# Kernel tuning notes

Measured on AMD Instinct MI355X. Metric: run time of the kernel, lower is better.

## Reference

```python
import jax, jax.numpy as jnp
import numpy as np

L, B, T, E, NH, HD, HID, V = 8, 2, 2048, 1024, 16, 64, 2816, 32000


def _rmsnorm(x, w, eps=1e-6):
    return w * (x * jax.lax.rsqrt(jnp.mean(x * x, axis=-1, keepdims=True) + eps))


def _rope(x, cos, sin):
    # x: [B,H,T,D]; cos/sin: [1,1,T,D/2]
    x1, x2 = jnp.split(x, 2, axis=-1)
    return jnp.concatenate([x1 * cos - x2 * sin, x1 * sin + x2 * cos], axis=-1)


def setup_inputs() -> dict:
    key = jax.random.key(0)
    ks = jax.random.split(key, 7)
    s = 0.02
    return {
        "idx": jax.random.randint(ks[0], (B, T), 0, V),
        "tok_emb": jax.random.normal(ks[1], (V, E), dtype=jnp.float32) * s,
        "qkv_w": jax.random.normal(ks[2], (L, 3 * E, E), dtype=jnp.float32) * s,
        "proj_w": jax.random.normal(ks[3], (L, E, E), dtype=jnp.float32) * s,
        "w1": jax.random.normal(ks[4], (L, HID, E), dtype=jnp.float32) * s,
        "w2": jax.random.normal(ks[5], (L, HID, E), dtype=jnp.float32) * s,
        "w3": jax.random.normal(ks[6], (L, E, HID), dtype=jnp.float32) * s,
        "norm1_w": jnp.ones((L, E), dtype=jnp.float32),
        "norm2_w": jnp.ones((L, E), dtype=jnp.float32),
        "norm_f_w": jnp.ones((E,), dtype=jnp.float32),
    }


def reference(idx, tok_emb, qkv_w, proj_w, w1, w2, w3, norm1_w, norm2_w, norm_f_w):
    x = tok_emb[idx]  # [B,T,E]
    # RoPE cache (start_pos=0, no kv cache -> prefill path)
    half = HD // 2
    inv_freq = 1.0 / (10000.0 ** (jnp.arange(half, dtype=jnp.float32) / half))
    pos = jnp.arange(T, dtype=jnp.float32)
    freqs = pos[:, None] * inv_freq[None, :]  # [T, D/2]
    cos = jnp.cos(freqs)[None, None]
    sin = jnp.sin(freqs)[None, None]
    causal = jnp.tril(jnp.ones((T, T), dtype=bool))
    scale = 1.0 / np.sqrt(HD).astype(np.float32)

    for l in range(L):
        # attention block
        h = _rmsnorm(x, norm1_w[l])
        qkv = h @ qkv_w[l].T  # [B,T,3E]
        q, k, v = jnp.split(qkv, 3, axis=-1)
        q = q.reshape(B, T, NH, HD).transpose(0, 2, 1, 3)
        k = k.reshape(B, T, NH, HD).transpose(0, 2, 1, 3)
        v = v.reshape(B, T, NH, HD).transpose(0, 2, 1, 3)
        q = _rope(q, cos, sin)
        k = _rope(k, cos, sin)
        att = jnp.einsum('bhqd,bhkd->bhqk', q, k) * scale
        att = jnp.where(causal, att, -jnp.inf)
        att = jax.nn.softmax(att, axis=-1)
        o = jnp.einsum('bhqk,bhkd->bhqd', att, v)
        o = o.transpose(0, 2, 1, 3).reshape(B, T, E)
        x = x + o @ proj_w[l].T
        # SwiGLU MLP
        h = _rmsnorm(x, norm2_w[l])
        x = x + (jax.nn.silu(h @ w1[l].T) * (h @ w2[l].T)) @ w3[l].T

    x = _rmsnorm(x, norm_f_w)
    logits = x @ tok_emb.T  # tied lm_head
    return logits
```

## Files before the change

kernel.cpp:

```cpp
#include <hip/hip_runtime.h>

#define GLOBAL_AS __attribute__((address_space(1)))
#define LDS_AS __attribute__((address_space(3)))

typedef unsigned short u16;
typedef unsigned int u32;
typedef __attribute__((ext_vector_type(4))) float f32x4;
typedef __attribute__((ext_vector_type(8))) short bf16x8;

#define TT 2048
#define EE 1024
#define NHH 16
#define HDD 64
#define HIDD 2816
#define VV 32000
#define MM 4096

__device__ __forceinline__ u16 f2bf(float f) {
  u32 u = __builtin_bit_cast(u32, f);
  u += 0x7fffu + ((u >> 16) & 1u);
  return (u16)(u >> 16);
}
__device__ __forceinline__ float bf2f(u16 v) {
  return __builtin_bit_cast(float, (u32)v << 16);
}


__global__ __launch_bounds__(256) void castbf_k(const float* __restrict__ in,
                                                u16* __restrict__ o, long n4) {
  const long i = (long)blockIdx.x * 256 + threadIdx.x;
  if (i >= n4) return;
  const float4 v = ((const float4*)in)[i];
  ((uint2*)o)[i] = make_uint2((u32)f2bf(v.x) | ((u32)f2bf(v.y) << 16),
                              (u32)f2bf(v.z) | ((u32)f2bf(v.w) << 16));
}

__global__ void ropetab_k(float* __restrict__ cosT, float* __restrict__ sinT) {
  const int t = blockIdx.x, j = threadIdx.x;
  const float inv = powf(10000.0f, -(float)j * (1.0f / 32.0f));
  const float f = (float)t * inv;
  cosT[t * 32 + j] = cosf(f);
  sinT[t * 32 + j] = sinf(f);
}

__global__ __launch_bounds__(256) void embed_k(const int* __restrict__ idx,
                                               const float* __restrict__ temb,
                                               float* __restrict__ x) {
  const int row = blockIdx.x;
  const int id = idx[row];
  ((float4*)(x + (size_t)row * EE))[threadIdx.x] =
      ((const float4*)(temb + (size_t)id * EE))[threadIdx.x];
}

__global__ __launch_bounds__(256) void rmsnorm_k(const float* __restrict__ x,
                                                 const float* __restrict__ w,
                                                 u16* __restrict__ o) {
  __shared__ float red[4];
  const int row = blockIdx.x, tid = threadIdx.x;
  const float4 v = ((const float4*)(x + (size_t)row * EE))[tid];
  float ss = v.x * v.x + v.y * v.y + v.z * v.z + v.w * v.w;
#pragma unroll
  for (int off = 32; off; off >>= 1) ss += __shfl_xor(ss, off, 64);
  if ((tid & 63) == 0) red[tid >> 6] = ss;
  __syncthreads();
  const float inv = rsqrtf((red[0] + red[1] + red[2] + red[3]) * (1.0f / 1024.0f) + 1e-6f);
  const float4 wv = ((const float4*)w)[tid];
  const u32 lo = (u32)f2bf(v.x * inv * wv.x) | ((u32)f2bf(v.y * inv * wv.y) << 16);
  const u32 hi = (u32)f2bf(v.z * inv * wv.z) | ((u32)f2bf(v.w * inv * wv.w) << 16);
  ((uint2*)(o + (size_t)row * EE))[tid] = make_uint2(lo, hi);
}

template <int OUTBF>
__global__ __launch_bounds__(512, 2) void gemm256p(const u16* __restrict__ A,
                                                   const u16* __restrict__ Bw,
                                                   float* __restrict__ C,
                                                   u16* __restrict__ C16,
                                                   const u16* __restrict__ G,
                                                   int N, int K) {
  __shared__ u16 lds[2 * 32768];
  const int t = threadIdx.x;
  const int lane = t & 63;
  const int wid = t >> 6;
  const int wr = wid >> 2;
  const int wc = wid & 3;
  const int l15 = lane & 15, lg = lane >> 4;
  const int bid = blockIdx.x;
  const int row0 = (bid & 15) << 8;
  const int col0 = (bid >> 4) << 8;
  const int NT = K >> 6;

  const int sr = t >> 3;
  const int su8 = (((t & 7) ^ (sr & 7)) << 3);
  const int t8 = t << 3;
  const u16* aG[4];
#pragma unroll
  for (int ga = 0; ga < 4; ++ga)
    aG[ga] = A + (size_t)(row0 + ga * 64 + sr) * K + su8;
  const u16* bG[4];
#pragma unroll
  for (int gb = 0; gb < 4; ++gb) {
    const int q = (gb * 2 + (sr >> 5)) & 3;
    const int nh = gb >> 1;
    bG[gb] = Bw + (size_t)(col0 + q * 64 + nh * 32 + (sr & 31)) * K + su8;
  }

  const int u0 = ((lg ^ (l15 & 7)) << 3);
  const int u1 = (((4 | lg) ^ (l15 & 7)) << 3);
  const int arow = (wr * 128 + l15) << 6;
  const int brow = 16384 + ((wc * 32 + l15) << 6);

  f32x4 acc[8][4] = {};

#define STA(nb, ga, k0n)                                                              \
  __builtin_amdgcn_global_load_lds((const GLOBAL_AS void*)(aG[ga] + (k0n)),           \
                                   (LDS_AS void*)((nb) + (ga)*4096 + t8), 16, 0, 0)
#define STB(nb, gb, k0n)                                                              \
  __builtin_amdgcn_global_load_lds((const GLOBAL_AS void*)(bG[gb] + (k0n)),           \
                                   (LDS_AS void*)((nb) + 16384 + (gb)*4096 + t8), 16, 0, 0)

  {
    u16* nb = lds;
    STA(nb, 0, 0); STA(nb, 2, 0);
    STB(nb, 0, 0); STB(nb, 1, 0);
    STB(nb, 2, 0); STB(nb, 3, 0);
    STA(nb, 1, 0); STA(nb, 3, 0);
  }

  bf16x8 af[4][2], bl[2][2], bh[2][2];

  for (int kt = 0; kt < NT; ++kt) {
    const bool st = (kt + 1 < NT);
    const int k0n = (kt + 1) << 6;
    const u16* cb = lds + (kt & 1) * 32768;
    u16* nb = lds + ((kt + 1) & 1) * 32768;

    asm volatile("s_waitcnt vmcnt(4)" ::: "memory");
    __builtin_amdgcn_s_barrier();
#pragma unroll
    for (int mi = 0; mi < 4; ++mi) {
      af[mi][0] = *(const bf16x8*)&cb[arow + mi * 1024 + u0];
      af[mi][1] = *(const bf16x8*)&cb[arow + mi * 1024 + u1];
    }
#pragma unroll
    for (int ni = 0; ni < 2; ++ni) {
      bl[ni][0] = *(const bf16x8*)&cb[brow + ni * 1024 + u0];
      bl[ni][1] = *(const bf16x8*)&cb[brow + ni * 1024 + u1];
    }
    if (st) { STA(nb, 0, k0n); STA(nb, 2, k0n); }
    __builtin_amdgcn_s_setprio(1);
#pragma unroll
    for (int mi = 0; mi < 4; ++mi)
#pragma unroll
      for (int ni = 0; ni < 2; ++ni) {
        acc[mi][ni] = __builtin_amdgcn_mfma_f32_16x16x32_bf16(af[mi][0], bl[ni][0], acc[mi][ni], 0, 0, 0);
        acc[mi][ni] = __builtin_amdgcn_mfma_f32_16x16x32_bf16(af[mi][1], bl[ni][1], acc[mi][ni], 0, 0, 0);
      }
    __builtin_amdgcn_s_setprio(0);

    if (st) { asm volatile("s_waitcnt vmcnt(4)" ::: "memory"); }
    else    { asm volatile("s_waitcnt vmcnt(2)" ::: "memory"); }
    __builtin_amdgcn_s_barrier();
#pragma unroll
    for (int ni = 0; ni < 2; ++ni) {
      bh[ni][0] = *(const bf16x8*)&cb[brow + 8192 + ni * 1024 + u0];
      bh[ni][1] = *(const bf16x8*)&cb[brow + 8192 + ni * 1024 + u1];
    }
    if (st) { STB(nb, 0, k0n); STB(nb, 1, k0n); }
    __builtin_amdgcn_s_setprio(1);
#pragma unroll
    for (int mi = 0; mi < 4; ++mi)
#pragma unroll
      for (int ni = 0; ni < 2; ++ni) {
        acc[mi][2 + ni] = __builtin_amdgcn_mfma_f32_16x16x32_bf16(af[mi][0], bh[ni][0], acc[mi][2 + ni], 0, 0, 0);
        acc[mi][2 + ni] = __builtin_amdgcn_mfma_f32_16x16x32_bf16(af[mi][1], bh[ni][1], acc[mi][2 + ni], 0, 0, 0);
      }
    __builtin_amdgcn_s_setprio(0);

    if (st) { asm volatile("s_waitcnt vmcnt(4)" ::: "memory"); }
    else    { asm volatile("s_waitcnt vmcnt(0)" ::: "memory"); }
    __builtin_amdgcn_s_barrier();
#pragma unroll
    for (int mi = 0; mi < 4; ++mi) {
      af[mi][0] = *(const bf16x8*)&cb[arow + (4 + mi) * 1024 + u0];
      af[mi][1] = *(const bf16x8*)&cb[arow + (4 + mi) * 1024 + u1];
    }
    if (st) { STB(nb, 2, k0n); STB(nb, 3, k0n); }
    __builtin_amdgcn_s_setprio(1);
#pragma unroll
    for (int mi = 0; mi < 4; ++mi)
#pragma unroll
      for (int ni = 0; ni < 2; ++ni) {
        acc[4 + mi][2 + ni] = __builtin_amdgcn_mfma_f32_16x16x32_bf16(af[mi][0], bh[ni][0], acc[4 + mi][2 + ni], 0, 0, 0);
        acc[4 + mi][2 + ni] = __builtin_amdgcn_mfma_f32_16x16x32_bf16(af[mi][1], bh[ni][1], acc[4 + mi][2 + ni], 0, 0, 0);
      }
    __builtin_amdgcn_s_setprio(0);

    if (st) { STA(nb, 1, k0n); STA(nb, 3, k0n); }
    __builtin_amdgcn_s_setprio(1);
#pragma unroll
    for (int mi = 0; mi < 4; ++mi)
#pragma unroll
      for (int ni = 0; ni < 2; ++ni) {
        acc[4 + mi][ni] = __builtin_amdgcn_mfma_f32_16x16x32_bf16(af[mi][0], bl[ni][0], acc[4 + mi][ni], 0, 0, 0);
        acc[4 + mi][ni] = __builtin_amdgcn_mfma_f32_16x16x32_bf16(af[mi][1], bl[ni][1], acc[4 + mi][ni], 0, 0, 0);
      }
    __builtin_amdgcn_s_setprio(0);
  }
#undef STA
#undef STB

#pragma unroll
  for (int m = 0; m < 8; ++m) {
    const int row = row0 + wr * 128 + m * 16 + lg * 4;
#pragma unroll
    for (int n = 0; n < 4; ++n) {
      const int col = col0 + wc * 64 + n * 16 + l15;
#pragma unroll
      for (int r = 0; r < 4; ++r) {
        const size_t o = (size_t)(row + r) * N + col;
        if (OUTBF == 0) {
          C[o] = acc[m][n][r];
        } else if (OUTBF == 1) {
          C16[o] = f2bf(acc[m][n][r]);
        } else {
          const float g = bf2f(G[o]);
          C16[o] = f2bf(g / (1.0f + __expf(-g)) * acc[m][n][r]);
        }
      }
    }
  }
}

template <int OUTBF>
__global__ __launch_bounds__(512, 2) void gemm128n(const u16* __restrict__ A,
                                                   const u16* __restrict__ Bw,
                                                   float* __restrict__ C,
                                                   const float* __restrict__ R,
                                                   const float* __restrict__ cosT,
                                                   const float* __restrict__ sinT,
                                                   u16* __restrict__ Qb,
                                                   u16* __restrict__ Kb,
                                                   u16* __restrict__ Vtb,
                                                   int N, int K) {
  __shared__ u16 lds[4 * 8192];
  const int t = threadIdx.x;
  const int lane = t & 63;
  const int wid = t >> 6;
  const int wr = wid & 3;
  const int wc = wid >> 2;
  const int l15 = lane & 15, lg = lane >> 4;
  const int bid = blockIdx.x;
  const int row0 = (bid & 31) << 7;
  const int col0 = (bid >> 5) << 7;
  const int NT = K >> 5;

  const int rA = t >> 2;
  const int usw = (((t & 3) ^ ((t >> 3) & 3)) << 3);
  const u16* sA = A + (size_t)(row0 + rA) * K + usw;
  const u16* sB = Bw + (size_t)(col0 + rA) * K + usw;
  const int dst = t << 3;

  const int e8 = ((lg ^ ((l15 >> 1) & 3)) << 3);
  const int aoff = (wr * 32 + l15) * 32 + e8;
  const int boff = 4096 + (wc * 64 + l15) * 32 + e8;

  f32x4 acc[2][4] = {};

  auto stage = [&](int kt) {
    u16* base = &lds[(kt & 3) * 8192];
    const size_t ko = (size_t)kt * 32;
    __builtin_amdgcn_global_load_lds((const GLOBAL_AS void*)(sA + ko),
                                     (LDS_AS void*)(base + dst), 16, 0, 0);
    __builtin_amdgcn_global_load_lds((const GLOBAL_AS void*)(sB + ko),
                                     (LDS_AS void*)(base + 4096 + dst), 16, 0, 0);
  };

  stage(0);
  stage(1);
  stage(2);

  for (int kt = 0; kt < NT; ++kt) {
    const int rem = NT - 1 - kt;
    if (rem >= 2) {
      asm volatile("s_waitcnt vmcnt(4)" ::: "memory");
    } else if (rem == 1) {
      asm volatile("s_waitcnt vmcnt(2)" ::: "memory");
    } else {
      asm volatile("s_waitcnt vmcnt(0)" ::: "memory");
    }
    __builtin_amdgcn_s_barrier();
    if (kt + 3 < NT) stage(kt + 3);
    const u16* base = &lds[(kt & 3) * 8192];
    bf16x8 af[2], bfv[4];
#pragma unroll
    for (int m = 0; m < 2; ++m) af[m] = *(const bf16x8*)&base[aoff + m * 512];
#pragma unroll
    for (int n = 0; n < 4; ++n) bfv[n] = *(const bf16x8*)&base[boff + n * 512];
    __builtin_amdgcn_s_setprio(1);
#pragma unroll
    for (int m = 0; m < 2; ++m)
#pragma unroll
      for (int n = 0; n < 4; ++n)
        acc[m][n] = __builtin_amdgcn_mfma_f32_16x16x32_bf16(af[m], bfv[n], acc[m][n], 0, 0, 0);
    __builtin_amdgcn_s_setprio(0);
  }

  if (OUTBF == 3) {
    const int reg = col0 >> 10;
    const int fb = col0 & 1023;
#pragma unroll
    for (int m = 0; m < 2; ++m) {
      const int row = row0 + wr * 32 + m * 16 + lg * 4;
      const int b = row >> 11, tbase = row & 2047;
      if (reg < 2) {
        u16* dstp = (reg == 0) ? Qb : Kb;
        const float qs = (reg == 0) ? 0.18033688011112042f : 1.0f;
#pragma unroll
        for (int n = 0; n < 2; ++n) {
          const int f = fb + wc * 64 + n * 16 + l15;
          const int h = f >> 6, j = f & 63;
#pragma unroll
          for (int r = 0; r < 4; ++r) {
            const int tt = tbase + r;
            const float c = cosT[tt * 32 + j], s = sinT[tt * 32 + j];
            const float x1 = acc[m][n][r], x2 = acc[m][n | 2][r];
            const size_t ro = ((size_t)(b * NHH + h) * TT + tt) * HDD + j;
            dstp[ro] = f2bf((x1 * c - x2 * s) * qs);
            dstp[ro + 32] = f2bf((x1 * s + x2 * c) * qs);
          }
        }
      } else {
#pragma unroll
        for (int n = 0; n < 4; ++n) {
          const int f = fb + wc * 64 + n * 16 + l15;
          const int h = f >> 6, j = f & 63;
          ushort4 pk;
          pk.x = f2bf(acc[m][n][0]);
          pk.y = f2bf(acc[m][n][1]);
          pk.z = f2bf(acc[m][n][2]);
          pk.w = f2bf(acc[m][n][3]);
          *(ushort4*)&Vtb[((size_t)(b * NHH + h) * HDD + j) * TT + tbase] = pk;
        }
      }
    }
    return;
  }

#pragma unroll
  for (int m = 0; m < 2; ++m) {
    const int row = row0 + wr * 32 + m * 16 + lg * 4;
#pragma unroll
    for (int n = 0; n < 4; ++n) {
      const int col = col0 + wc * 64 + n * 16 + l15;
#pragma unroll
      for (int r = 0; r < 4; ++r) {
        const size_t o = (size_t)(row + r) * N + col;
        C[o] = acc[m][n][r] + R[o];
      }
    }
  }
}

__global__ __launch_bounds__(512, 2) void gemm128d(const u16* __restrict__ A,
                                                   const u16* __restrict__ Bg,
                                                   const u16* __restrict__ Bu,
                                                   u16* __restrict__ C16,
                                                   int N, int K) {
  __shared__ u16 lds[3 * 8192];
  const int t = threadIdx.x;
  const int lane = t & 63;
  const int wid = t >> 6;
  const int wr = wid & 3;
  const int wc = wid >> 2;
  const int l15 = lane & 15, lg = lane >> 4;
  const int bid = blockIdx.x;
  const int row0 = (bid & 31) << 7;
  const int col0 = (bid >> 5) << 6;
  const int NT = K >> 5;

  const int rA = t >> 2;
  const int usw = (((t & 3) ^ ((t >> 3) & 3)) << 3);
  const u16* sA = A + (size_t)(row0 + rA) * K + usw;
  const int tb = t & 255;
  const int rB = tb >> 2;
  const int uswB = (((tb & 3) ^ ((tb >> 3) & 3)) << 3);
  const u16* sB = ((wid < 4) ? Bg : Bu) + (size_t)(col0 + rB) * K + uswB;
  const int dstA = t << 3;
  const int dstB = 4096 + ((wid < 4) ? 0 : 2048) + (tb << 3);

  const int e8 = ((lg ^ ((l15 >> 1) & 3)) << 3);
  const int aoff = (wr * 32 + l15) * 32 + e8;
  const int goff = 4096 + (wc * 32 + l15) * 32 + e8;
  const int uoff = 6144 + (wc * 32 + l15) * 32 + e8;

  f32x4 ag[2][2] = {}, au[2][2] = {};

  auto stage = [&](int kt, int buf) {
    u16* b = &lds[buf * 8192];
    const size_t ko = (size_t)kt * 32;
    __builtin_amdgcn_global_load_lds((const GLOBAL_AS void*)(sA + ko),
                                     (LDS_AS void*)(b + dstA), 16, 0, 0);
    __builtin_amdgcn_global_load_lds((const GLOBAL_AS void*)(sB + ko),
                                     (LDS_AS void*)(b + dstB), 16, 0, 0);
  };

  stage(0, 0);
  stage(1, 1);

  int cbuf = 0;
  for (int kt = 0; kt < NT; ++kt) {
    if (kt + 1 < NT) {
      asm volatile("s_waitcnt vmcnt(2)" ::: "memory");
    } else {
      asm volatile("s_waitcnt vmcnt(0)" ::: "memory");
    }
    __builtin_amdgcn_s_barrier();
    const int nbuf = (cbuf == 2) ? 0 : cbuf + 1;
    const int sbuf = (nbuf == 2) ? 0 : nbuf + 1;
    if (kt + 2 < NT) stage(kt + 2, sbuf);
    const u16* cb = &lds[cbuf * 8192];
    bf16x8 af[2], bgv[2], buv[2];
#pragma unroll
    for (int m = 0; m < 2; ++m) af[m] = *(const bf16x8*)&cb[aoff + m * 512];
#pragma unroll
    for (int n = 0; n < 2; ++n) {
      bgv[n] = *(const bf16x8*)&cb[goff + n * 512];
      buv[n] = *(const bf16x8*)&cb[uoff + n * 512];
    }
    __builtin_amdgcn_s_setprio(1);
#pragma unroll
    for (int m = 0; m < 2; ++m)
#pragma unroll
      for (int n = 0; n < 2; ++n) {
        ag[m][n] = __builtin_amdgcn_mfma_f32_16x16x32_bf16(af[m], bgv[n], ag[m][n], 0, 0, 0);
        au[m][n] = __builtin_amdgcn_mfma_f32_16x16x32_bf16(af[m], buv[n], au[m][n], 0, 0, 0);
      }
    __builtin_amdgcn_s_setprio(0);
    cbuf = nbuf;
  }

#pragma unroll
  for (int m = 0; m < 2; ++m) {
    const int row = row0 + wr * 32 + m * 16 + lg * 4;
#pragma unroll
    for (int n = 0; n < 2; ++n) {
      const int col = col0 + wc * 32 + n * 16 + l15;
#pragma unroll
      for (int r = 0; r < 4; ++r) {
        const float g = ag[m][n][r];
        const float u = au[m][n][r];
        C16[(size_t)(row + r) * N + col] = f2bf(g / (1.0f + __expf(-g)) * u);
      }
    }
  }
}

__global__ __launch_bounds__(256) void attn_k(const u16* __restrict__ Q,
                                              const u16* __restrict__ Kc,
                                              const u16* __restrict__ Vt,
                                              u16* __restrict__ O) {
  __shared__ u16 P_lds[4][32][72];
  const int bid = blockIdx.x;
  const int bh = bid & 31;
  const int jj = bid >> 5;
  const int qi = (bid < 256) ? jj : 23 - jj;
  const int q0 = qi << 7;
  const int lane = threadIdx.x & 63;
  const int w = threadIdx.x >> 6;
  const int l15 = lane & 15, lg = lane >> 4;
  const int qbase = q0 + w * 32;

  bf16x8 qf[2][2];
#pragma unroll
  for (int am = 0; am < 2; ++am)
#pragma unroll
    for (int ks = 0; ks < 2; ++ks)
      qf[am][ks] = *(const bf16x8*)&Q[((size_t)bh * TT + qbase + am * 16 + l15) * HDD + ks * 32 + lg * 8];

  bf16x8 ones;
#pragma unroll
  for (int i = 0; i < 8; ++i) ones[i] = (short)0x3F80;

  f32x4 oacc[2][4] = {};
  f32x4 lacc[2] = {};

  const int ntile = (q0 + 128) >> 6;
  for (int kt = 0; kt < ntile; ++kt) {
    const int k0 = kt << 6;
    f32x4 s[2][4];
    bf16x8 kf0[4], kf1[4];
#pragma unroll
    for (int an = 0; an < 4; ++an) {
      kf0[an] = *(const bf16x8*)&Kc[((size_t)bh * TT + k0 + an * 16 + l15) * HDD + lg * 8];
      kf1[an] = *(const bf16x8*)&Kc[((size_t)bh * TT + k0 + an * 16 + l15) * HDD + 32 + lg * 8];
    }
    __builtin_amdgcn_s_setprio(1);
#pragma unroll
    for (int an = 0; an < 4; ++an) {
#pragma unroll
      for (int am = 0; am < 2; ++am) {
        f32x4 z = {0.0f, 0.0f, 0.0f, 0.0f};
        z = __builtin_amdgcn_mfma_f32_16x16x32_bf16(qf[am][0], kf0[an], z, 0, 0, 0);
        s[am][an] = __builtin_amdgcn_mfma_f32_16x16x32_bf16(qf[am][1], kf1[an], z, 0, 0, 0);
      }
    }
    __builtin_amdgcn_s_setprio(0);
    const bool diag = (k0 + 64) > q0;
#pragma unroll
    for (int am = 0; am < 2; ++am)
#pragma unroll
      for (int an = 0; an < 4; ++an)
#pragma unroll
        for (int r = 0; r < 4; ++r) {
          float v = s[am][an][r];
          if (diag) {
            const int qrow = qbase + am * 16 + lg * 4 + r;
            const int kcol = k0 + an * 16 + l15;
            if (kcol > qrow) v = -1e30f;
          }
          float p;
          asm("v_exp_f32 %0, %1" : "=v"(p) : "v"(v));
          s[am][an][r] = p;
        }
#pragma unroll
    for (int am = 0; am < 2; ++am)
#pragma unroll
      for (int an = 0; an < 4; ++an)
#pragma unroll
        for (int rp = 0; rp < 2; ++rp) {
          u32 pk;
          asm("v_cvt_pk_bf16_f32 %0, %1, %2"
              : "=v"(pk) : "v"(s[am][an][2 * rp]), "v"(s[am][an][2 * rp + 1]));
          const int rowb = am * 16 + lg * 4 + 2 * rp;
          P_lds[w][rowb][an * 16 + l15] = (u16)pk;
          P_lds[w][rowb + 1][an * 16 + l15] = (u16)(pk >> 16);
        }
#pragma unroll
    for (int ks = 0; ks < 2; ++ks) {
      bf16x8 pf[2];
#pragma unroll
      for (int am = 0; am < 2; ++am)
        pf[am] = *(const bf16x8*)&P_lds[w][am * 16 + l15][ks * 32 + lg * 8];
      __builtin_amdgcn_s_setprio(1);
#pragma unroll
      for (int dn = 0; dn < 4; ++dn) {
        const bf16x8 vf = *(const bf16x8*)&Vt[((size_t)bh * HDD + dn * 16 + l15) * TT + k0 + ks * 32 + lg * 8];
#pragma unroll
        for (int am = 0; am < 2; ++am)
          oacc[am][dn] = __builtin_amdgcn_mfma_f32_16x16x32_bf16(pf[am], vf, oacc[am][dn], 0, 0, 0);
      }
#pragma unroll
      for (int am = 0; am < 2; ++am)
        lacc[am] = __builtin_amdgcn_mfma_f32_16x16x32_bf16(pf[am], ones, lacc[am], 0, 0, 0);
      __builtin_amdgcn_s_setprio(0);
    }
  }
  const int b = bh >> 4, h = bh & 15;
#pragma unroll
  for (int am = 0; am < 2; ++am)
#pragma unroll
    for (int r = 0; r < 4; ++r) {
      const float il = 1.0f / lacc[am][r];
      const int qrow = qbase + am * 16 + lg * 4 + r;
#pragma unroll
      for (int dn = 0; dn < 4; ++dn)
        O[((size_t)b * TT + qrow) * EE + h * 64 + dn * 16 + l15] = f2bf(oacc[am][dn][r] * il);
    }
}


extern "C" void kernel_launch(void* const* d_in, const int* in_sizes, int n_in,
                              void* d_out, int out_size, void* d_ws, size_t ws_size,
                              hipStream_t stream) {
  const int* idx = (const int*)d_in[0];
  const float* tok_emb = (const float*)d_in[1];
  const float* qkv_w = (const float*)d_in[2];
  const float* proj_w = (const float*)d_in[3];
  const float* w1 = (const float*)d_in[4];
  const float* w2 = (const float*)d_in[5];
  const float* w3 = (const float*)d_in[6];
  const float* norm1_w = (const float*)d_in[7];
  const float* norm2_w = (const float*)d_in[8];
  const float* norm_f_w = (const float*)d_in[9];
  float* out = (float*)d_out;

  char* ws = (char*)d_ws;
  size_t off = 0;
  auto alloc = [&](size_t bytes) -> void* {
    off = (off + 255) & ~(size_t)255;
    void* p = ws + off;
    off += bytes;
    return p;
  };

  const size_t N_TEMB = (size_t)VV * EE;
  const size_t N_QKVW = (size_t)8 * 3 * EE * EE;
  const size_t N_PROJW = (size_t)8 * EE * EE;
  const size_t N_W1 = (size_t)8 * HIDD * EE;
  const size_t N_W3 = (size_t)8 * EE * HIDD;

  u16* tembbf = (u16*)alloc(N_TEMB * 2);
  u16* qkvwbf = (u16*)alloc(N_QKVW * 2);
  u16* projwbf = (u16*)alloc(N_PROJW * 2);
  u16* w1bf = (u16*)alloc(N_W1 * 2);
  u16* w2bf = (u16*)alloc(N_W1 * 2);
  u16* w3bf = (u16*)alloc(N_W3 * 2);
  float* x = (float*)alloc((size_t)MM * EE * 4);
  u16* h1 = (u16*)alloc((size_t)MM * EE * 2);
  u16* hg = (u16*)alloc((size_t)MM * HIDD * 2);
  u16* qb = (u16*)alloc((size_t)2 * NHH * TT * HDD * 2);
  u16* kb = (u16*)alloc((size_t)2 * NHH * TT * HDD * 2);
  u16* vtb = (u16*)alloc((size_t)2 * NHH * TT * HDD * 2);
  u16* attno = (u16*)alloc((size_t)MM * EE * 2);
  float* cosT = (float*)alloc((size_t)TT * 32 * 4);
  float* sinT = (float*)alloc((size_t)TT * 32 * 4);

  auto cast = [&](const float* src, u16* dst, size_t n) {
    const long n4 = (long)(n / 4);
    castbf_k<<<(int)((n4 + 255) / 256), 256, 0, stream>>>(src, dst, n4);
  };
  cast(tok_emb, tembbf, N_TEMB);
  cast(qkv_w, qkvwbf, N_QKVW);
  cast(proj_w, projwbf, N_PROJW);
  cast(w1, w1bf, N_W1);
  cast(w2, w2bf, N_W1);
  cast(w3, w3bf, N_W3);

  ropetab_k<<<TT, 32, 0, stream>>>(cosT, sinT);
  embed_k<<<MM, 256, 0, stream>>>(idx, tok_emb, x);

  for (int l = 0; l < 8; ++l) {
    rmsnorm_k<<<MM, 256, 0, stream>>>(x, norm1_w + l * EE, h1);
    gemm128n<3><<<dim3(24 * 32), 512, 0, stream>>>(h1, qkvwbf + (size_t)l * 3 * EE * EE,
                                                   nullptr, nullptr,
                                                   cosT, sinT, qb, kb, vtb, 3 * EE, EE);
    attn_k<<<dim3(512), 256, 0, stream>>>(qb, kb, vtb, attno);
    gemm128n<0><<<dim3(8 * 32), 512, 0, stream>>>(attno, projwbf + (size_t)l * EE * EE,
                                                  x, x,
                                                  nullptr, nullptr, nullptr, nullptr, nullptr,
                                                  EE, EE);
    rmsnorm_k<<<MM, 256, 0, stream>>>(x, norm2_w + l * EE, h1);
    gemm128d<<<dim3(44 * 32), 512, 0, stream>>>(h1, w1bf + (size_t)l * HIDD * EE,
                                                w2bf + (size_t)l * HIDD * EE,
                                                hg, HIDD, EE);
    gemm128n<0><<<dim3(8 * 32), 512, 0, stream>>>(hg, w3bf + (size_t)l * EE * HIDD,
                                                  x, x,
                                                  nullptr, nullptr, nullptr, nullptr, nullptr,
                                                  EE, HIDD);
  }
  rmsnorm_k<<<MM, 256, 0, stream>>>(x, norm_f_w, h1);
  gemm256p<0><<<dim3(125 * 16), 512, 0, stream>>>(h1, tembbf, out, nullptr, nullptr,
                                                  VV, EE);
}
```

Baseline: 2.420 ms.

## Replace LM-head GEMM with 256x128 tile, K=32 steps and higher occupancy

```diff
diff --git a/kernel.cpp b/kernel.cpp
--- a/kernel.cpp
+++ b/kernel.cpp
@@ -70,163 +70,95 @@
   ((uint2*)(o + (size_t)row * EE))[tid] = make_uint2(lo, hi);
 }
 
-template <int OUTBF>
-__global__ __launch_bounds__(512, 2) void gemm256p(const u16* __restrict__ A,
+__global__ __launch_bounds__(512, 4) void gemm256x(const u16* __restrict__ A,
                                                    const u16* __restrict__ Bw,
                                                    float* __restrict__ C,
-                                                   u16* __restrict__ C16,
-                                                   const u16* __restrict__ G,
                                                    int N, int K) {
-  __shared__ u16 lds[2 * 32768];
+  __shared__ u16 lds[2 * 12288];
   const int t = threadIdx.x;
   const int lane = t & 63;
-  const int wid = t >> 6;
-  const int wr = wid >> 2;
-  const int wc = wid & 3;
+  const int w = t >> 6;
+  const int wr = w >> 1;
+  const int wc = w & 1;
   const int l15 = lane & 15, lg = lane >> 4;
   const int bid = blockIdx.x;
   const int row0 = (bid & 15) << 8;
-  const int col0 = (bid >> 4) << 8;
-  const int NT = K >> 6;
-
-  const int sr = t >> 3;
-  const int su8 = (((t & 7) ^ (sr & 7)) << 3);
-  const int t8 = t << 3;
-  const u16* aG[4];
-#pragma unroll
-  for (int ga = 0; ga < 4; ++ga)
-    aG[ga] = A + (size_t)(row0 + ga * 64 + sr) * K + su8;
-  const u16* bG[4];
-#pragma unroll
-  for (int gb = 0; gb < 4; ++gb) {
-    const int q = (gb * 2 + (sr >> 5)) & 3;
-    const int nh = gb >> 1;
-    bG[gb] = Bw + (size_t)(col0 + q * 64 + nh * 32 + (sr & 31)) * K + su8;
-  }
-
-  const int u0 = ((lg ^ (l15 & 7)) << 3);
-  const int u1 = (((4 | lg) ^ (l15 & 7)) << 3);
-  const int arow = (wr * 128 + l15) << 6;
-  const int brow = 16384 + ((wc * 32 + l15) << 6);
-
-  f32x4 acc[8][4] = {};
-
-#define STA(nb, ga, k0n)                                                              \
-  __builtin_amdgcn_global_load_lds((const GLOBAL_AS void*)(aG[ga] + (k0n)),           \
-                                   (LDS_AS void*)((nb) + (ga)*4096 + t8), 16, 0, 0)
-#define STB(nb, gb, k0n)                                                              \
-  __builtin_amdgcn_global_load_lds((const GLOBAL_AS void*)(bG[gb] + (k0n)),           \
-                                   (LDS_AS void*)((nb) + 16384 + (gb)*4096 + t8), 16, 0, 0)
-
-  {
-    u16* nb = lds;
-    STA(nb, 0, 0); STA(nb, 2, 0);
-    STB(nb, 0, 0); STB(nb, 1, 0);
-    STB(nb, 2, 0); STB(nb, 3, 0);
-    STA(nb, 1, 0); STA(nb, 3, 0);
-  }
-
-  bf16x8 af[4][2], bl[2][2], bh[2][2];
+  const int col0 = (bid >> 4) << 7;
+  const int NT = K >> 5;
+
+  const int gsw = (((lane & 3) ^ ((lane >> 2) & 3) ^ (lane >> 4)) << 3);
+  const u16* srcA1 = A + (size_t)(row0 + (w >> 1) * 64 + (w & 1) * 16 + (lane >> 2)) * K + gsw;
+  const u16* srcA2 = srcA1 + (size_t)32 * K;
+  const u16* srcB = Bw + (size_t)(col0 + w * 16 + (lane >> 2)) * K + gsw;
+  const int dA1 = (w >> 1) * 1024 + (w & 1) * 512 + lane * 8;
+  const int dB = 8192 + w * 512 + lane * 8;
+
+  const int usw = ((lg ^ (l15 & 3) ^ ((l15 >> 2) & 3)) << 3);
+  const int abase = wr * 1024 + l15 * 32 + usw;
+  const int bbase = 8192 + wc * 2048 + l15 * 32 + usw;
+
+  f32x4 acc[4][4] = {};
+
+  auto sA1 = [&](int kt, u16* nb) {
+    __builtin_amdgcn_global_load_lds((const GLOBAL_AS void*)(srcA1 + (size_t)kt * 32),
+                                     (LDS_AS void*)(nb + dA1), 16, 0, 0);
+  };
+  auto sA2 = [&](int kt, u16* nb) {
+    __builtin_amdgcn_global_load_lds((const GLOBAL_AS void*)(srcA2 + (size_t)kt * 32),
+                                     (LDS_AS void*)(nb + dA1 + 4096), 16, 0, 0);
+  };
+  auto sB = [&](int kt, u16* nb) {
+    __builtin_amdgcn_global_load_lds((const GLOBAL_AS void*)(srcB + (size_t)kt * 32),
+                                     (LDS_AS void*)(nb + dB), 16, 0, 0);
+  };
+
+  sA1(0, lds); sB(0, lds); sA2(0, lds);
 
   for (int kt = 0; kt < NT; ++kt) {
     const bool st = (kt + 1 < NT);
-    const int k0n = (kt + 1) << 6;
-    const u16* cb = lds + (kt & 1) * 32768;
-    u16* nb = lds + ((kt + 1) & 1) * 32768;
-
-    asm volatile("s_waitcnt vmcnt(4)" ::: "memory");
+    u16* cb = lds + (kt & 1) * 12288;
+    u16* nb = lds + ((kt + 1) & 1) * 12288;
+    bf16x8 af[4], bfv[4];
+
+    asm volatile("s_waitcnt vmcnt(1)" ::: "memory");
     __builtin_amdgcn_s_barrier();
 #pragma unroll
-    for (int mi = 0; mi < 4; ++mi) {
-      af[mi][0] = *(const bf16x8*)&cb[arow + mi * 1024 + u0];
-      af[mi][1] = *(const bf16x8*)&cb[arow + mi * 1024 + u1];
-    }
-#pragma unroll
-    for (int ni = 0; ni < 2; ++ni) {
-      bl[ni][0] = *(const bf16x8*)&cb[brow + ni * 1024 + u0];
-      bl[ni][1] = *(const bf16x8*)&cb[brow + ni * 1024 + u1];
-    }
-    if (st) { STA(nb, 0, k0n); STA(nb, 2, k0n); }
+    for (int mi = 0; mi < 2; ++mi) af[mi] = *(const bf16x8*)&cb[abase + mi * 512];
+#pragma unroll
+    for (int n = 0; n < 4; ++n) bfv[n] = *(const bf16x8*)&cb[bbase + n * 512];
+    if (st) { sA1(kt + 1, nb); sB(kt + 1, nb); }
     __builtin_amdgcn_s_setprio(1);
 #pragma unroll
-    for (int mi = 0; mi < 4; ++mi)
-#pragma unroll
-      for (int ni = 0; ni < 2; ++ni) {
-        acc[mi][ni] = __builtin_amdgcn_mfma_f32_16x16x32_bf16(af[mi][0], bl[ni][0], acc[mi][ni], 0, 0, 0);
-        acc[mi][ni] = __builtin_amdgcn_mfma_f32_16x16x32_bf16(af[mi][1], bl[ni][1], acc[mi][ni], 0, 0, 0);
-      }
+    for (int mi = 0; mi < 2; ++mi)
+#pragma unroll
+      for (int n = 0; n < 4; ++n)
+        acc[mi][n] = __builtin_amdgcn_mfma_f32_16x16x32_bf16(af[mi], bfv[n], acc[mi][n], 0, 0, 0);
     __builtin_amdgcn_s_setprio(0);
 
-    if (st) { asm volatile("s_waitcnt vmcnt(4)" ::: "memory"); }
-    else    { asm volatile("s_waitcnt vmcnt(2)" ::: "memory"); }
-    __builtin_amdgcn_s_barrier();
-#pragma unroll
-    for (int ni = 0; ni < 2; ++ni) {
-      bh[ni][0] = *(const bf16x8*)&cb[brow + 8192 + ni * 1024 + u0];
-      bh[ni][1] = *(const bf16x8*)&cb[brow + 8192 + ni * 1024 + u1];
-    }
-    if (st) { STB(nb, 0, k0n); STB(nb, 1, k0n); }
-    __builtin_amdgcn_s_setprio(1);
-#pragma unroll
-    for (int mi = 0; mi < 4; ++mi)
-#pragma unroll
-      for (int ni = 0; ni < 2; ++ni) {
-        acc[mi][2 + ni] = __builtin_amdgcn_mfma_f32_16x16x32_bf16(af[mi][0], bh[ni][0], acc[mi][2 + ni], 0, 0, 0);
-        acc[mi][2 + ni] = __builtin_amdgcn_mfma_f32_16x16x32_bf16(af[mi][1], bh[ni][1], acc[mi][2 + ni], 0, 0, 0);
-      }
-    __builtin_amdgcn_s_setprio(0);
-
-    if (st) { asm volatile("s_waitcnt vmcnt(4)" ::: "memory"); }
+    if (st) { asm volatile("s_waitcnt vmcnt(2)" ::: "memory"); }
     else    { asm volatile("s_waitcnt vmcnt(0)" ::: "memory"); }
     __builtin_amdgcn_s_barrier();
 #pragma unroll
-    for (int mi = 0; mi < 4; ++mi) {
-      af[mi][0] = *(const bf16x8*)&cb[arow + (4 + mi) * 1024 + u0];
-      af[mi][1] = *(const bf16x8*)&cb[arow + (4 + mi) * 1024 + u1];
-    }
-    if (st) { STB(nb, 2, k0n); STB(nb, 3, k0n); }
+    for (int mi = 0; mi < 2; ++mi) af[2 + mi] = *(const bf16x8*)&cb[abase + 4096 + mi * 512];
+    if (st) sA2(kt + 1, nb);
     __builtin_amdgcn_s_setprio(1);
 #pragma unroll
-    for (int mi = 0; mi < 4; ++mi)
-#pragma unroll
-      for (int ni = 0; ni < 2; ++ni) {
-        acc[4 + mi][2 + ni] = __builtin_amdgcn_mfma_f32_16x16x32_bf16(af[mi][0], bh[ni][0], acc[4 + mi][2 + ni], 0, 0, 0);
-        acc[4 + mi][2 + ni] = __builtin_amdgcn_mfma_f32_16x16x32_bf16(af[mi][1], bh[ni][1], acc[4 + mi][2 + ni], 0, 0, 0);
-      }
+    for (int mi = 0; mi < 2; ++mi)
+#pragma unroll
+      for (int n = 0; n < 4; ++n)
+        acc[2 + mi][n] = __builtin_amdgcn_mfma_f32_16x16x32_bf16(af[2 + mi], bfv[n], acc[2 + mi][n], 0, 0, 0);
     __builtin_amdgcn_s_setprio(0);
-
-    if (st) { STA(nb, 1, k0n); STA(nb, 3, k0n); }
-    __builtin_amdgcn_s_setprio(1);
-#pragma unroll
-    for (int mi = 0; mi < 4; ++mi)
-#pragma unroll
-      for (int ni = 0; ni < 2; ++ni) {
-        acc[4 + mi][ni] = __builtin_amdgcn_mfma_f32_16x16x32_bf16(af[mi][0], bl[ni][0], acc[4 + mi][ni], 0, 0, 0);
-        acc[4 + mi][ni] = __builtin_amdgcn_mfma_f32_16x16x32_bf16(af[mi][1], bl[ni][1], acc[4 + mi][ni], 0, 0, 0);
-      }
-    __builtin_amdgcn_s_setprio(0);
-  }
-#undef STA
-#undef STB
-
-#pragma unroll
-  for (int m = 0; m < 8; ++m) {
-    const int row = row0 + wr * 128 + m * 16 + lg * 4;
+  }
+
+#pragma unroll
+  for (int m = 0; m < 4; ++m) {
+    const int row = row0 + wr * 64 + m * 16 + lg * 4;
 #pragma unroll
     for (int n = 0; n < 4; ++n) {
       const int col = col0 + wc * 64 + n * 16 + l15;
 #pragma unroll
-      for (int r = 0; r < 4; ++r) {
-        const size_t o = (size_t)(row + r) * N + col;
-        if (OUTBF == 0) {
-          C[o] = acc[m][n][r];
-        } else if (OUTBF == 1) {
-          C16[o] = f2bf(acc[m][n][r]);
-        } else {
-          const float g = bf2f(G[o]);
-          C16[o] = f2bf(g / (1.0f + __expf(-g)) * acc[m][n][r]);
-        }
-      }
+      for (int r = 0; r < 4; ++r)
+        C[(size_t)(row + r) * N + col] = acc[m][n][r];
     }
   }
 }
@@ -649,6 +581,5 @@
                                                   EE, HIDD);
   }
   rmsnorm_k<<<MM, 256, 0, stream>>>(x, norm_f_w, h1);
-  gemm256p<0><<<dim3(125 * 16), 512, 0, stream>>>(h1, tembbf, out, nullptr, nullptr,
-                                                  VV, EE);
-}
+  gemm256x<<<dim3(250 * 16), 512, 0, stream>>>(h1, tembbf, out, VV, EE);
+}
```

Result: no change. 2.454 ms (+1.4%).
